# Optimization experiments

Hardware: AMD Instinct MI355X
Metric: run time of the kernel (lower is better)

The kernel has to match this reference:

```python
import jax, jax.numpy as jnp
import numpy as np

def setup_inputs() -> dict:
    key = jax.random.key(0)
    k1, k2, k3 = jax.random.split(key, 3)
    N, C, H, W = 16, 128, 128, 128
    out_chn = 128
    x = jax.random.normal(k1, (N, C, H, W), dtype=jnp.float32)
    # 1x1 conv = per-pixel linear: weight (out_chn, in_chn), bias (out_chn,)
    fan_in = C  # kernel_size=1 -> fan_in = in_chn
    bound = 1.0 / np.sqrt(fan_in)
    conv_w = jax.random.uniform(k2, (out_chn, C), dtype=jnp.float32, minval=-bound, maxval=bound)
    conv_b = jax.random.uniform(k3, (out_chn,), dtype=jnp.float32, minval=-bound, maxval=bound)
    return {"x": x, "conv_w": conv_w, "conv_b": conv_b}

def reference(x, conv_w, conv_b):
    N, C, H, W = x.shape
    x_hw = x.reshape(N, C, H * W)                     # (N, C, HW)
    logits = jnp.einsum('ncl,ndl->ncd', x_hw, x_hw)    # (N, C, C), unscaled
    weights = jax.nn.softmax(logits, axis=-1)
    attn = jnp.einsum('ncd,ndl->ncl', weights, x_hw)   # (N, C, HW)
    attn = attn.reshape(N, C, H, W)
    # 1x1 conv: contract over channel dim
    out = jnp.einsum('nchw,oc->nohw', attn, conv_w) + conv_b[None, :, None, None]
    return out
```

## Files before the change

kernel.cpp:

```cpp
#include <hip/hip_runtime.h>
#include <hip/hip_bf16.h>
#include <stdint.h>

#define NB    16
#define CD    128
#define HW    16384

typedef float  f32x4  __attribute__((ext_vector_type(4)));
typedef short  bf16x8 __attribute__((ext_vector_type(8)));

__device__ __forceinline__ unsigned short f2bf(float f) {
    unsigned u = __float_as_uint(f);
    u += 0x7FFFu + ((u >> 16) & 1u);
    return (unsigned short)(u >> 16);
}

__global__ __launch_bounds__(256) void gram_kernel(const float* __restrict__ x,
                                                   float* __restrict__ G) {
    const int n  = blockIdx.x;
    const int kc = blockIdx.y;
    const int t    = threadIdx.x;
    const int wv   = t >> 6;
    const int lane = t & 63;
    const int q    = lane >> 4;
    const int r16  = lane & 15;

    __shared__ __align__(16) unsigned short Xl[CD * 132];

    f32x4 acc[4][4];
#pragma unroll
    for (int i = 0; i < 4; ++i)
#pragma unroll
        for (int j = 0; j < 4; ++j) acc[i][j] = (f32x4)0.0f;

    const int rt0 = 4 * (wv >> 1);
    const int ct0 = 4 * (wv & 1);

    const float* xb = x + (size_t)n * CD * HW;

    for (int sub = 0; sub < 8; ++sub) {
        const int kbase = kc * 1024 + sub * 128;
#pragma unroll
        for (int i = 0; i < 16; ++i) {
            int f  = i * 256 + t;
            int c  = f >> 5;
            int l4 = (f & 31) * 4;
            float4 v = *(const float4*)(xb + (size_t)c * HW + kbase + l4);
            uint2 pk;
            pk.x = (unsigned)f2bf(v.x) | ((unsigned)f2bf(v.y) << 16);
            pk.y = (unsigned)f2bf(v.z) | ((unsigned)f2bf(v.w) << 16);
            *(uint2*)(&Xl[c * 132 + l4]) = pk;
        }
        __syncthreads();

#pragma unroll
        for (int ks = 0; ks < 4; ++ks) {
            const int k0 = ks * 32 + q * 8;
            bf16x8 af[4], bfr[4];
#pragma unroll
            for (int i = 0; i < 4; ++i) {
                const unsigned short* pa = &Xl[(16 * (rt0 + i) + r16) * 132 + k0];
                union { bf16x8 v; uint2 u[2]; } ua;
                ua.u[0] = *(const uint2*)pa;
                ua.u[1] = *(const uint2*)(pa + 4);
                af[i] = ua.v;
                const unsigned short* pb = &Xl[(16 * (ct0 + i) + r16) * 132 + k0];
                union { bf16x8 v; uint2 u[2]; } ub;
                ub.u[0] = *(const uint2*)pb;
                ub.u[1] = *(const uint2*)(pb + 4);
                bfr[i] = ub.v;
            }
#pragma unroll
            for (int i = 0; i < 4; ++i)
#pragma unroll
                for (int j = 0; j < 4; ++j)
                    acc[i][j] = __builtin_amdgcn_mfma_f32_16x16x32_bf16(
                        af[i], bfr[j], acc[i][j], 0, 0, 0);
        }
        __syncthreads();
    }

    float* Gn = G + (size_t)n * CD * CD;
#pragma unroll
    for (int i = 0; i < 4; ++i)
#pragma unroll
        for (int j = 0; j < 4; ++j)
#pragma unroll
            for (int rr = 0; rr < 4; ++rr) {
                int row = 16 * (rt0 + i) + q * 4 + rr;
                int col = 16 * (ct0 + j) + r16;
                atomicAdd(&Gn[row * CD + col], acc[i][j][rr]);
            }
}

__global__ __launch_bounds__(256) void rowstats_kernel(const float* __restrict__ G,
                                                       float* __restrict__ mx,
                                                       float* __restrict__ rs) {
    const int row  = blockIdx.x * 4 + (threadIdx.x >> 6);
    const int lane = threadIdx.x & 63;
    const float* g = G + (size_t)row * CD;
    float g0 = g[lane];
    float g1 = g[lane + 64];
    float m = fmaxf(g0, g1);
#pragma unroll
    for (int off = 32; off > 0; off >>= 1) m = fmaxf(m, __shfl_xor(m, off));
    float s = __expf(g0 - m) + __expf(g1 - m);
#pragma unroll
    for (int off = 32; off > 0; off >>= 1) s += __shfl_xor(s, off);
    if (lane == 0) {
        mx[row] = m;
        rs[row] = 1.0f / s;
    }
}

__global__ __launch_bounds__(256) void mmat_kernel(const float* __restrict__ G,
                                                   const float* __restrict__ mx,
                                                   const float* __restrict__ rs,
                                                   const float* __restrict__ cw,
                                                   unsigned short* __restrict__ Mbf) {
    const int n  = blockIdx.x;
    const int bo = blockIdx.y;
    const int t  = threadIdx.x;
    __shared__ __align__(16) float Wl[CD * CD];

    const float* Gn  = G  + (size_t)n * CD * CD;
    const float* mxn = mx + n * CD;
    const float* rsn = rs + n * CD;

#pragma unroll 4
    for (int i = 0; i < 64; ++i) {
        int e = i * 256 + t;
        int c = e >> 7;
        int d = e & 127;
        Wl[c * CD + d] = __expf(Gn[c * CD + d] - mxn[c]) * rsn[c];
    }
    __syncthreads();

    const int o  = bo * 16 + (t >> 4);
    const int d0 = (t & 15) * 8;
    float a0 = 0, a1 = 0, a2 = 0, a3 = 0, a4 = 0, a5 = 0, a6 = 0, a7 = 0;
    const float* cwo = cw + (size_t)o * CD;
#pragma unroll 4
    for (int c = 0; c < CD; ++c) {
        float cv = cwo[c];
        float4 w0 = *(const float4*)&Wl[c * CD + d0];
        float4 w1 = *(const float4*)&Wl[c * CD + d0 + 4];
        a0 += cv * w0.x; a1 += cv * w0.y; a2 += cv * w0.z; a3 += cv * w0.w;
        a4 += cv * w1.x; a5 += cv * w1.y; a6 += cv * w1.z; a7 += cv * w1.w;
    }
    uint4 pk;
    pk.x = (unsigned)f2bf(a0) | ((unsigned)f2bf(a1) << 16);
    pk.y = (unsigned)f2bf(a2) | ((unsigned)f2bf(a3) << 16);
    pk.z = (unsigned)f2bf(a4) | ((unsigned)f2bf(a5) << 16);
    pk.w = (unsigned)f2bf(a6) | ((unsigned)f2bf(a7) << 16);
    *(uint4*)&Mbf[((size_t)n * CD + o) * CD + d0] = pk;
}

__global__ __launch_bounds__(256) void out_kernel(const float* __restrict__ x,
                                                  const unsigned short* __restrict__ Mbf,
                                                  const float* __restrict__ bias,
                                                  float* __restrict__ out) {
    const int lb = blockIdx.x;
    const int n  = blockIdx.y;
    const int l0 = lb * 128;
    const int t    = threadIdx.x;
    const int wv   = t >> 6;
    const int lane = t & 63;
    const int q    = lane >> 4;
    const int r16  = lane & 15;

    __shared__ __align__(16) unsigned short Xt[128 * 132];
    __shared__ float bl[CD];

    const int ot0 = 4 * (wv >> 1);
    const int lt0 = 4 * (wv & 1);

    bf16x8 af[4][4];
    const unsigned short* Mn = Mbf + (size_t)n * CD * CD;
#pragma unroll
    for (int i = 0; i < 4; ++i)
#pragma unroll
        for (int ks = 0; ks < 4; ++ks) {
            int o = 16 * (ot0 + i) + r16;
            int k = ks * 32 + q * 8;
            union { bf16x8 v; uint4 u; } ua;
            ua.u = *(const uint4*)(&Mn[o * CD + k]);
            af[i][ks] = ua.v;
        }

    if (t < CD) bl[t] = bias[t];

    const float* xb = x + (size_t)n * CD * HW + l0;
#pragma unroll
    for (int i = 0; i < 16; ++i) {
        int f  = i * 256 + t;
        int d  = f >> 5;
        int l4 = (f & 31) * 4;
        float4 v = *(const float4*)(xb + (size_t)d * HW + l4);
        Xt[(l4 + 0) * 132 + d] = f2bf(v.x);
        Xt[(l4 + 1) * 132 + d] = f2bf(v.y);
        Xt[(l4 + 2) * 132 + d] = f2bf(v.z);
        Xt[(l4 + 3) * 132 + d] = f2bf(v.w);
    }
    __syncthreads();

    f32x4 acc[4][4];
#pragma unroll
    for (int i = 0; i < 4; ++i)
#pragma unroll
        for (int j = 0; j < 4; ++j) acc[i][j] = (f32x4)0.0f;

#pragma unroll
    for (int ks = 0; ks < 4; ++ks) {
        bf16x8 bfr[4];
#pragma unroll
        for (int j = 0; j < 4; ++j) {
            const unsigned short* pb = &Xt[(16 * (lt0 + j) + r16) * 132 + ks * 32 + q * 8];
            union { bf16x8 v; uint2 u[2]; } ub;
            ub.u[0] = *(const uint2*)pb;
            ub.u[1] = *(const uint2*)(pb + 4);
            bfr[j] = ub.v;
        }
#pragma unroll
        for (int i = 0; i < 4; ++i)
#pragma unroll
            for (int j = 0; j < 4; ++j)
                acc[i][j] = __builtin_amdgcn_mfma_f32_16x16x32_bf16(
                    af[i][ks], bfr[j], acc[i][j], 0, 0, 0);
    }

    float* ob = out + (size_t)n * CD * HW + l0;
#pragma unroll
    for (int i = 0; i < 4; ++i)
#pragma unroll
        for (int j = 0; j < 4; ++j)
#pragma unroll
            for (int rr = 0; rr < 4; ++rr) {
                int o = 16 * (ot0 + i) + q * 4 + rr;
                int l = 16 * (lt0 + j) + r16;
                ob[(size_t)o * HW + l] = acc[i][j][rr] + bl[o];
            }
}

extern "C" void kernel_launch(void* const* d_in, const int* in_sizes, int n_in,
                              void* d_out, int out_size, void* d_ws, size_t ws_size,
                              hipStream_t stream) {
    const float* x  = (const float*)d_in[0];
    const float* cw = (const float*)d_in[1];
    const float* cb = (const float*)d_in[2];
    float* out = (float*)d_out;

    char* ws = (char*)d_ws;
    float*          G   = (float*)(ws);
    float*          mxp = (float*)(ws + (1u << 20));
    float*          rsp = (float*)(ws + (1u << 20) + 8192);
    unsigned short* Mbf = (unsigned short*)(ws + (1u << 20) + 16384);

    hipMemsetAsync(G, 0, (size_t)NB * CD * CD * sizeof(float), stream);

    gram_kernel   <<<dim3(NB, 16), 256, 0, stream>>>(x, G);
    rowstats_kernel<<<dim3(512),    256, 0, stream>>>(G, mxp, rsp);
    mmat_kernel   <<<dim3(NB, 8),  256, 0, stream>>>(G, mxp, rsp, cw, Mbf);
    out_kernel    <<<dim3(128, NB), 256, 0, stream>>>(x, Mbf, cb, out);
}
```

Baseline: 307.7 us.

## Split gram K-range across more blocks and restructure out_kernel transpose with swizzled LDS

The gram kernel now launches 64 K-chunks per batch instead of 16, each covering 256 columns, so four times as many blocks run and each does less serial work. It relies on the existing atomic accumulation into G, which now receives more atomics. The output kernel swaps the MFMA operand roles so pixels are the A operand and the M matrix is B. It also transposes x into LDS using packed 4-channel uint2 writes with an XOR swizzle instead of scalar padded stores, and reads fragments with single 16-byte loads. Stores become float4 vectors along the pixel dimension, replacing scalar strided stores.

```diff
diff --git a/kernel.cpp b/kernel.cpp
--- a/kernel.cpp
+++ b/kernel.cpp
@@ -9,10 +9,10 @@
 typedef float  f32x4  __attribute__((ext_vector_type(4)));
 typedef short  bf16x8 __attribute__((ext_vector_type(8)));
 
-__device__ __forceinline__ unsigned short f2bf(float f) {
+__device__ __forceinline__ unsigned f2bf(float f) {
     unsigned u = __float_as_uint(f);
     u += 0x7FFFu + ((u >> 16) & 1u);
-    return (unsigned short)(u >> 16);
+    return u >> 16;
 }
 
 __global__ __launch_bounds__(256) void gram_kernel(const float* __restrict__ x,
@@ -38,8 +38,8 @@
 
     const float* xb = x + (size_t)n * CD * HW;
 
-    for (int sub = 0; sub < 8; ++sub) {
-        const int kbase = kc * 1024 + sub * 128;
+    for (int sub = 0; sub < 2; ++sub) {
+        const int kbase = kc * 256 + sub * 128;
 #pragma unroll
         for (int i = 0; i < 16; ++i) {
             int f  = i * 256 + t;
@@ -47,8 +47,8 @@
             int l4 = (f & 31) * 4;
             float4 v = *(const float4*)(xb + (size_t)c * HW + kbase + l4);
             uint2 pk;
-            pk.x = (unsigned)f2bf(v.x) | ((unsigned)f2bf(v.y) << 16);
-            pk.y = (unsigned)f2bf(v.z) | ((unsigned)f2bf(v.w) << 16);
+            pk.x = f2bf(v.x) | (f2bf(v.y) << 16);
+            pk.y = f2bf(v.z) | (f2bf(v.w) << 16);
             *(uint2*)(&Xl[c * 132 + l4]) = pk;
         }
         __syncthreads();
@@ -149,10 +149,10 @@
         a4 += cv * w1.x; a5 += cv * w1.y; a6 += cv * w1.z; a7 += cv * w1.w;
     }
     uint4 pk;
-    pk.x = (unsigned)f2bf(a0) | ((unsigned)f2bf(a1) << 16);
-    pk.y = (unsigned)f2bf(a2) | ((unsigned)f2bf(a3) << 16);
-    pk.z = (unsigned)f2bf(a4) | ((unsigned)f2bf(a5) << 16);
-    pk.w = (unsigned)f2bf(a6) | ((unsigned)f2bf(a7) << 16);
+    pk.x = f2bf(a0) | (f2bf(a1) << 16);
+    pk.y = f2bf(a2) | (f2bf(a3) << 16);
+    pk.z = f2bf(a4) | (f2bf(a5) << 16);
+    pk.w = f2bf(a6) | (f2bf(a7) << 16);
     *(uint4*)&Mbf[((size_t)n * CD + o) * CD + d0] = pk;
 }
 
@@ -169,77 +169,90 @@
     const int q    = lane >> 4;
     const int r16  = lane & 15;
 
-    __shared__ __align__(16) unsigned short Xt[128 * 132];
+    __shared__ __align__(16) unsigned short Xt[128 * 128];
     __shared__ float bl[CD];
 
-    const int ot0 = 4 * (wv >> 1);
-    const int lt0 = 4 * (wv & 1);
-
-    bf16x8 af[4][4];
+    const int lt0 = 4 * (wv >> 1);
+    const int ot0 = 4 * (wv & 1);
+
+    if (t < CD) bl[t] = bias[t];
+
+    const float* xb = x + (size_t)n * CD * HW + l0;
+    const int lt = t & 31;
+    const int dg = t >> 5;
+#pragma unroll
+    for (int i = 0; i < 4; ++i) {
+        const int d0 = i * 32 + dg * 4;
+        const float* bp = xb + (size_t)d0 * HW + 4 * lt;
+        float4 v0 = *(const float4*)(bp);
+        float4 v1 = *(const float4*)(bp + HW);
+        float4 v2 = *(const float4*)(bp + 2 * HW);
+        float4 v3 = *(const float4*)(bp + 3 * HW);
+        float r0[4] = {v0.x, v0.y, v0.z, v0.w};
+        float r1[4] = {v1.x, v1.y, v1.z, v1.w};
+        float r2[4] = {v2.x, v2.y, v2.z, v2.w};
+        float r3[4] = {v3.x, v3.y, v3.z, v3.w};
+        const int dph = d0 ^ (8 * (lt & 7));
+#pragma unroll
+        for (int j = 0; j < 4; ++j) {
+            uint2 pk;
+            pk.x = f2bf(r0[j]) | (f2bf(r1[j]) << 16);
+            pk.y = f2bf(r2[j]) | (f2bf(r3[j]) << 16);
+            *(uint2*)&Xt[(4 * lt + j) * 128 + dph] = pk;
+        }
+    }
+    __syncthreads();
+
+    f32x4 acc[4][4];
+#pragma unroll
+    for (int i = 0; i < 4; ++i)
+#pragma unroll
+        for (int j = 0; j < 4; ++j) acc[i][j] = (f32x4)0.0f;
+
     const unsigned short* Mn = Mbf + (size_t)n * CD * CD;
 #pragma unroll
-    for (int i = 0; i < 4; ++i)
-#pragma unroll
-        for (int ks = 0; ks < 4; ++ks) {
-            int o = 16 * (ot0 + i) + r16;
-            int k = ks * 32 + q * 8;
+    for (int ks = 0; ks < 4; ++ks) {
+        const int k0 = ks * 32 + q * 8;
+        bf16x8 bfr[4];
+#pragma unroll
+        for (int j = 0; j < 4; ++j) {
+            const int o = 16 * (ot0 + j) + r16;
+            union { bf16x8 v; uint4 u; } ub;
+            ub.u = *(const uint4*)&Mn[o * CD + k0];
+            bfr[j] = ub.v;
+        }
+        bf16x8 af[4];
+#pragma unroll
+        for (int i = 0; i < 4; ++i) {
+            const int l = 16 * (lt0 + i) + r16;
+            const int doff = k0 ^ (8 * ((l >> 2) & 7));
             union { bf16x8 v; uint4 u; } ua;
-            ua.u = *(const uint4*)(&Mn[o * CD + k]);
-            af[i][ks] = ua.v;
-        }
-
-    if (t < CD) bl[t] = bias[t];
-
-    const float* xb = x + (size_t)n * CD * HW + l0;
-#pragma unroll
-    for (int i = 0; i < 16; ++i) {
-        int f  = i * 256 + t;
-        int d  = f >> 5;
-        int l4 = (f & 31) * 4;
-        float4 v = *(const float4*)(xb + (size_t)d * HW + l4);
-        Xt[(l4 + 0) * 132 + d] = f2bf(v.x);
-        Xt[(l4 + 1) * 132 + d] = f2bf(v.y);
-        Xt[(l4 + 2) * 132 + d] = f2bf(v.z);
-        Xt[(l4 + 3) * 132 + d] = f2bf(v.w);
-    }
-    __syncthreads();
-
-    f32x4 acc[4][4];
-#pragma unroll
-    for (int i = 0; i < 4; ++i)
-#pragma unroll
-        for (int j = 0; j < 4; ++j) acc[i][j] = (f32x4)0.0f;
-
-#pragma unroll
-    for (int ks = 0; ks < 4; ++ks) {
-        bf16x8 bfr[4];
-#pragma unroll
-        for (int j = 0; j < 4; ++j) {
-            const unsigned short* pb = &Xt[(16 * (lt0 + j) + r16) * 132 + ks * 32 + q * 8];
-            union { bf16x8 v; uint2 u[2]; } ub;
-            ub.u[0] = *(const uint2*)pb;
-            ub.u[1] = *(const uint2*)(pb + 4);
-            bfr[j] = ub.v;
+            ua.u = *(const uint4*)&Xt[l * 128 + doff];
+            af[i] = ua.v;
         }
 #pragma unroll
         for (int i = 0; i < 4; ++i)
 #pragma unroll
             for (int j = 0; j < 4; ++j)
                 acc[i][j] = __builtin_amdgcn_mfma_f32_16x16x32_bf16(
-                    af[i][ks], bfr[j], acc[i][j], 0, 0, 0);
+                    af[i], bfr[j], acc[i][j], 0, 0, 0);
     }
 
     float* ob = out + (size_t)n * CD * HW + l0;
 #pragma unroll
     for (int i = 0; i < 4; ++i)
 #pragma unroll
-        for (int j = 0; j < 4; ++j)
-#pragma unroll
-            for (int rr = 0; rr < 4; ++rr) {
-                int o = 16 * (ot0 + i) + q * 4 + rr;
-                int l = 16 * (lt0 + j) + r16;
-                ob[(size_t)o * HW + l] = acc[i][j][rr] + bl[o];
-            }
+        for (int j = 0; j < 4; ++j) {
+            const int o = 16 * (ot0 + j) + r16;
+            const int l = 16 * (lt0 + i) + q * 4;
+            const float b = bl[o];
+            float4 st;
+            st.x = acc[i][j][0] + b;
+            st.y = acc[i][j][1] + b;
+            st.z = acc[i][j][2] + b;
+            st.w = acc[i][j][3] + b;
+            *(float4*)(ob + (size_t)o * HW + l) = st;
+        }
 }
 
 extern "C" void kernel_launch(void* const* d_in, const int* in_sizes, int n_in,
@@ -258,8 +271,8 @@
 
     hipMemsetAsync(G, 0, (size_t)NB * CD * CD * sizeof(float), stream);
 
-    gram_kernel   <<<dim3(NB, 16), 256, 0, stream>>>(x, G);
+    gram_kernel    <<<dim3(NB, 64), 256, 0, stream>>>(x, G);
     rowstats_kernel<<<dim3(512),    256, 0, stream>>>(G, mxp, rsp);
-    mmat_kernel   <<<dim3(NB, 8),  256, 0, stream>>>(G, mxp, rsp, cw, Mbf);
-    out_kernel    <<<dim3(128, NB), 256, 0, stream>>>(x, Mbf, cb, out);
-}
+    mmat_kernel    <<<dim3(NB, 8),  256, 0, stream>>>(G, mxp, rsp, cw, Mbf);
+    out_kernel     <<<dim3(128, NB), 256, 0, stream>>>(x, Mbf, cb, out);
+}
```

New measurement: 340.9 us. 1.11x slower.
